# Kernel optimization log

Measured on AMD Instinct MI355X. Metric: run time of the kernel, lower is better.

## Reference

```python
import jax, jax.numpy as jnp
import numpy as np

D = 1024
HEADS = 16
HEAD_DIM = D // HEADS
B = 4
L = 1024


def setup_inputs() -> dict:
    key = jax.random.key(0)
    kq, kk, kv, kw, kb = jax.random.split(key, 5)
    Q = jax.random.normal(kq, (B, L, D), dtype=jnp.float32)
    K = jax.random.normal(kk, (B, L, D), dtype=jnp.float32)
    V = jax.random.normal(kv, (B, L, D), dtype=jnp.float32)
    # Output projection H: torch nn.Linear(D, D) -> weight (D, D), bias (D,)
    lim = 1.0 / np.sqrt(D)
    W_H = jax.random.uniform(kw, (D, D), minval=-lim, maxval=lim, dtype=jnp.float32)
    b_H = jax.random.uniform(kb, (D,), minval=-lim, maxval=lim, dtype=jnp.float32)
    mask = 0  # falsy -> no masking branch, matching `if mask` in the source
    return {"Q": Q, "K": K, "V": V, "W_H": W_H, "b_H": b_H, "mask": mask}


def reference(Q, K, V, W_H, b_H, mask):
    batch, q_len, _ = Q.shape
    k_len = K.shape[1]
    Qh = Q.reshape(batch, q_len, HEADS, HEAD_DIM)
    Kh = K.reshape(batch, k_len, HEADS, HEAD_DIM)
    Vh = V.reshape(batch, k_len, HEADS, HEAD_DIM)
    scores = jnp.einsum('bqhd,bkhd->bhqk', Qh, Kh)  # [B,H,Lq,Lk]
    if mask:  # mask is a Python scalar (0 -> skip), as in source
        scores = jnp.where(mask == 0, -jnp.inf, scores)
    # NOTE: source scales by sqrt(D), not sqrt(head_dim)
    attn = jax.nn.softmax(scores / np.sqrt(D).astype(np.float32), axis=3)
    out = jnp.einsum('bhql,blhd->bqhd', attn, Vh).reshape(batch, q_len, D)
    return out @ W_H.T + b_H
```

## Files before the change

kernel.cpp:

```cpp
#include <hip/hip_runtime.h>
#include <hip/hip_bf16.h>

typedef __attribute__((ext_vector_type(4))) float f32x4;
typedef __attribute__((ext_vector_type(8))) short bf16x8;

constexpr int Bn  = 4;
constexpr int Ln  = 1024;
constexpr int Dn  = 1024;
constexpr int Hn  = 16;
constexpr int HDn = 64;

static __device__ __forceinline__ unsigned short bf16r(float f) {
    union { float f; unsigned int u; } x;
    x.f = f;
    unsigned int r = x.u + 0x7fffu + ((x.u >> 16) & 1u);
    return (unsigned short)(r >> 16);
}

__global__ __launch_bounds__(256) void prep_kernel(
    const float* __restrict__ Kg, const float* __restrict__ Vg,
    const float* __restrict__ Wg, unsigned short* __restrict__ Kbf,
    unsigned short* __restrict__ Vtg, unsigned short* __restrict__ Wbf)
{
    const int tid = threadIdx.x;
    if (blockIdx.z == 4) {
        const int r0 = blockIdx.x * 64, c0 = blockIdx.y * 64;
        for (int i = 0; i < 4; ++i) {
            int e4 = i * 256 + tid;
            int r = e4 >> 4, c4 = e4 & 15;
            const float* p = Wg + (size_t)(r0 + r) * Dn + c0 + c4 * 4;
            float4 v = *(const float4*)p;
            ushort4 o;
            o.x = bf16r(v.x); o.y = bf16r(v.y); o.z = bf16r(v.z); o.w = bf16r(v.w);
            *(ushort4*)(Wbf + (size_t)(r0 + r) * Dn + c0 + c4 * 4) = o;
        }
        return;
    }

    __shared__ unsigned short T[64][72];
    const int k0 = blockIdx.x * 64;
    const int h  = blockIdx.y;
    const int b  = blockIdx.z;
    const float* Kb = Kg + (size_t)b * Ln * Dn + h * HDn;
    const float* Vb = Vg + (size_t)b * Ln * Dn + h * HDn;
    unsigned short* Ko = Kbf + (size_t)b * Ln * Dn + h * HDn;

    for (int i = 0; i < 4; ++i) {
        int e4 = i * 256 + tid;
        int r = e4 >> 4, c4 = e4 & 15;
        float4 kv = *(const float4*)(Kb + (size_t)(k0 + r) * Dn + c4 * 4);
        ushort4 o;
        o.x = bf16r(kv.x); o.y = bf16r(kv.y); o.z = bf16r(kv.z); o.w = bf16r(kv.w);
        *(ushort4*)(Ko + (size_t)(k0 + r) * Dn + c4 * 4) = o;
        float4 vv = *(const float4*)(Vb + (size_t)(k0 + r) * Dn + c4 * 4);
        T[c4 * 4 + 0][r] = bf16r(vv.x);
        T[c4 * 4 + 1][r] = bf16r(vv.y);
        T[c4 * 4 + 2][r] = bf16r(vv.z);
        T[c4 * 4 + 3][r] = bf16r(vv.w);
    }
    __syncthreads();
    unsigned short* out = Vtg + ((size_t)(b * Hn + h) * HDn) * Ln + k0;
    for (int i = 0; i < 2; ++i) {
        int e8 = i * 256 + tid;
        int r = e8 >> 3, c8 = e8 & 7;
        *(uint4*)(out + (size_t)r * Ln + c8 * 8) = *(const uint4*)&T[r][c8 * 8];
    }
}

__global__ __launch_bounds__(512) void attn_kernel(
    const float* __restrict__ Qg, const unsigned short* __restrict__ Kbf,
    const unsigned short* __restrict__ Vtg, unsigned short* __restrict__ Xg)
{
    __shared__ unsigned short Ks[64][72];
    __shared__ unsigned short Vts[64][72];
    __shared__ unsigned short Ps[128][72];

    const int tid  = threadIdx.x;
    const int wave = tid >> 6;
    const int lane = tid & 63;
    const int l16  = lane & 15;
    const int quad = lane >> 4;

    const int q0 = blockIdx.x * 128;
    const int h  = blockIdx.y;
    const int b  = blockIdx.z;

    const unsigned short* Kb16 = Kbf + (size_t)b * Ln * Dn + h * HDn;
    const unsigned short* Vtb  = Vtg + ((size_t)(b * Hn + h) * HDn) * Ln;

    bf16x8 aq0, aq1;
    {
        const float* qp = Qg + ((size_t)b * Ln + q0 + wave * 16 + l16) * Dn
                             + h * HDn + quad * 8;
        float4 a0 = *(const float4*)qp;
        float4 a1 = *(const float4*)(qp + 4);
        float4 a2 = *(const float4*)(qp + 32);
        float4 a3 = *(const float4*)(qp + 36);
        aq0[0] = (short)bf16r(a0.x); aq0[1] = (short)bf16r(a0.y);
        aq0[2] = (short)bf16r(a0.z); aq0[3] = (short)bf16r(a0.w);
        aq0[4] = (short)bf16r(a1.x); aq0[5] = (short)bf16r(a1.y);
        aq0[6] = (short)bf16r(a1.z); aq0[7] = (short)bf16r(a1.w);
        aq1[0] = (short)bf16r(a2.x); aq1[1] = (short)bf16r(a2.y);
        aq1[2] = (short)bf16r(a2.z); aq1[3] = (short)bf16r(a2.w);
        aq1[4] = (short)bf16r(a3.x); aq1[5] = (short)bf16r(a3.y);
        aq1[6] = (short)bf16r(a3.z); aq1[7] = (short)bf16r(a3.w);
    }

    const float SC = 1.4426950408889634f / 32.0f;

    float lsum[4] = {0.f, 0.f, 0.f, 0.f};
    f32x4 Oacc[4];
    for (int d = 0; d < 4; ++d) Oacc[d] = (f32x4){0.f, 0.f, 0.f, 0.f};

    for (int it = 0; it < Ln / 64; ++it) {
        const int k0 = it * 64;
        __syncthreads();
        {
            int r = tid >> 3, c8 = tid & 7;
            *(uint4*)&Ks[r][c8 * 8] =
                *(const uint4*)(Kb16 + (size_t)(k0 + r) * Dn + c8 * 8);
            *(uint4*)&Vts[r][c8 * 8] =
                *(const uint4*)(Vtb + (size_t)r * Ln + k0 + c8 * 8);
        }
        __syncthreads();

        f32x4 s[4];
        for (int n = 0; n < 4; ++n) {
            bf16x8 b0 = *(const bf16x8*)&Ks[n * 16 + l16][quad * 8];
            bf16x8 b1 = *(const bf16x8*)&Ks[n * 16 + l16][32 + quad * 8];
            f32x4 acc = (f32x4){0.f, 0.f, 0.f, 0.f};
            acc = __builtin_amdgcn_mfma_f32_16x16x32_bf16(aq0, b0, acc, 0, 0, 0);
            acc = __builtin_amdgcn_mfma_f32_16x16x32_bf16(aq1, b1, acc, 0, 0, 0);
            s[n] = acc;
        }

        for (int n = 0; n < 4; ++n)
            for (int r = 0; r < 4; ++r) {
                float p = exp2f(s[n][r] * SC);
                s[n][r] = p;
                lsum[r] += p;
            }

        for (int n = 0; n < 4; ++n)
            for (int r = 0; r < 4; ++r)
                Ps[wave * 16 + quad * 4 + r][n * 16 + l16] = bf16r(s[n][r]);

        for (int kk = 0; kk < 2; ++kk) {
            bf16x8 ap = *(const bf16x8*)&Ps[wave * 16 + l16][kk * 32 + quad * 8];
            for (int d = 0; d < 4; ++d) {
                bf16x8 bv = *(const bf16x8*)&Vts[d * 16 + l16][kk * 32 + quad * 8];
                Oacc[d] = __builtin_amdgcn_mfma_f32_16x16x32_bf16(ap, bv, Oacc[d], 0, 0, 0);
            }
        }
    }

    float linv[4];
    for (int r = 0; r < 4; ++r) {
        float rs = lsum[r];
        rs += __shfl_xor(rs, 1, 64);
        rs += __shfl_xor(rs, 2, 64);
        rs += __shfl_xor(rs, 4, 64);
        rs += __shfl_xor(rs, 8, 64);
        linv[r] = 1.f / rs;
    }

    unsigned short* Xb = Xg + ((size_t)b * Ln + q0) * Dn + h * HDn;
    for (int r = 0; r < 4; ++r) {
        int row = wave * 16 + quad * 4 + r;
        for (int d = 0; d < 4; ++d)
            Xb[(size_t)row * Dn + d * 16 + l16] = bf16r(Oacc[d][r] * linv[r]);
    }
}

__global__ __launch_bounds__(256) void proj_kernel(
    const unsigned short* __restrict__ Xg, const unsigned short* __restrict__ Wbf,
    const float* __restrict__ bg, float* __restrict__ Yg)
{
    __shared__ unsigned short Xs[64][136];
    __shared__ unsigned short Wsh[64][136];

    const int tid  = threadIdx.x;
    const int wave = tid >> 6;
    const int lane = tid & 63;
    const int l16  = lane & 15;
    const int quad = lane >> 4;
    const int mw   = (wave & 1) * 32;
    const int nw   = (wave >> 1) * 32;

    const int m0 = blockIdx.x * 64;
    const int n0 = blockIdx.y * 64;

    f32x4 acc[2][2];
    for (int mt = 0; mt < 2; ++mt)
        for (int nt = 0; nt < 2; ++nt)
            acc[mt][nt] = (f32x4){0.f, 0.f, 0.f, 0.f};

    for (int it = 0; it < Dn / 128; ++it) {
        const int kk0 = it * 128;
        __syncthreads();
        for (int i = 0; i < 4; ++i) {
            int idx = i * 256 + tid;
            int r = idx >> 4, c8 = idx & 15;
            *(uint4*)&Xs[r][c8 * 8] =
                *(const uint4*)(Xg + (size_t)(m0 + r) * Dn + kk0 + c8 * 8);
            *(uint4*)&Wsh[r][c8 * 8] =
                *(const uint4*)(Wbf + (size_t)(n0 + r) * Dn + kk0 + c8 * 8);
        }
        __syncthreads();

        for (int kk = 0; kk < 4; ++kk) {
            bf16x8 af[2], bfr[2];
            for (int mt = 0; mt < 2; ++mt)
                af[mt] = *(const bf16x8*)&Xs[mw + mt * 16 + l16][kk * 32 + quad * 8];
            for (int nt = 0; nt < 2; ++nt)
                bfr[nt] = *(const bf16x8*)&Wsh[nw + nt * 16 + l16][kk * 32 + quad * 8];
            for (int mt = 0; mt < 2; ++mt)
                for (int nt = 0; nt < 2; ++nt)
                    acc[mt][nt] = __builtin_amdgcn_mfma_f32_16x16x32_bf16(
                        af[mt], bfr[nt], acc[mt][nt], 0, 0, 0);
        }
    }

    for (int nt = 0; nt < 2; ++nt) {
        int col = n0 + nw + nt * 16 + l16;
        float bb = bg[col];
        for (int mt = 0; mt < 2; ++mt)
            for (int r = 0; r < 4; ++r) {
                int row = m0 + mw + mt * 16 + quad * 4 + r;
                Yg[(size_t)row * Dn + col] = acc[mt][nt][r] + bb;
            }
    }
}

extern "C" void kernel_launch(void* const* d_in, const int* in_sizes, int n_in,
                              void* d_out, int out_size, void* d_ws, size_t ws_size,
                              hipStream_t stream) {
    const float* Q    = (const float*)d_in[0];
    const float* K    = (const float*)d_in[1];
    const float* V    = (const float*)d_in[2];
    const float* W    = (const float*)d_in[3];
    const float* bias = (const float*)d_in[4];

    unsigned short* Kbf = (unsigned short*)d_ws;
    unsigned short* Vt  = Kbf + (size_t)Bn * Ln * Dn;
    unsigned short* Wbf = Vt  + (size_t)Bn * Ln * Dn;
    unsigned short* X   = Wbf + (size_t)Dn * Dn;
    float* Y = (float*)d_out;

    dim3 gp(Ln / 64, Hn, Bn + 1);
    prep_kernel<<<gp, 256, 0, stream>>>(K, V, W, Kbf, Vt, Wbf);

    dim3 g1(Ln / 128, Hn, Bn);
    attn_kernel<<<g1, 512, 0, stream>>>(Q, Kbf, Vt, X);

    dim3 g2((Bn * Ln) / 64, Dn / 64);
    proj_kernel<<<g2, 256, 0, stream>>>(X, Wbf, bias, Y);
}
```

Before: 155.9 us.

## Keep P in registers via transposed QK MFMA; enlarge projection GEMM tiles

The attention kernel swaps the MFMA operands so the score fragments come out laid out as the A operand of a 16x16x16 MFMA. This lets P stay in registers and removes the shared-memory round trip and its bf16 writes, and it packs P to bf16 with perm instructions. The row sum now reduces across quads with fewer shuffles, and the grid order puts heads innermost. The projection GEMM moves to 128x128 tiles with 512 threads and a K step of 64, trading more per-wave accumulators and fewer blocks for more data reuse.

```diff
diff --git a/kernel.cpp b/kernel.cpp
--- a/kernel.cpp
+++ b/kernel.cpp
@@ -3,6 +3,13 @@
 
 typedef __attribute__((ext_vector_type(4))) float f32x4;
 typedef __attribute__((ext_vector_type(8))) short bf16x8;
+typedef __attribute__((ext_vector_type(4))) short bf16x4;
+
+#if __has_builtin(__builtin_amdgcn_mfma_f32_16x16x16_bf16)
+#define MFMA_16x16x16(a, b, c) __builtin_amdgcn_mfma_f32_16x16x16_bf16(a, b, c, 0, 0, 0)
+#else
+#define MFMA_16x16x16(a, b, c) __builtin_amdgcn_mfma_f32_16x16x16bf16_1k(a, b, c, 0, 0, 0)
+#endif
 
 constexpr int Bn  = 4;
 constexpr int Ln  = 1024;
@@ -28,8 +35,7 @@
         for (int i = 0; i < 4; ++i) {
             int e4 = i * 256 + tid;
             int r = e4 >> 4, c4 = e4 & 15;
-            const float* p = Wg + (size_t)(r0 + r) * Dn + c0 + c4 * 4;
-            float4 v = *(const float4*)p;
+            float4 v = *(const float4*)(Wg + (size_t)(r0 + r) * Dn + c0 + c4 * 4);
             ushort4 o;
             o.x = bf16r(v.x); o.y = bf16r(v.y); o.z = bf16r(v.z); o.w = bf16r(v.w);
             *(ushort4*)(Wbf + (size_t)(r0 + r) * Dn + c0 + c4 * 4) = o;
@@ -73,7 +79,6 @@
 {
     __shared__ unsigned short Ks[64][72];
     __shared__ unsigned short Vts[64][72];
-    __shared__ unsigned short Ps[128][72];
 
     const int tid  = threadIdx.x;
     const int wave = tid >> 6;
@@ -81,8 +86,8 @@
     const int l16  = lane & 15;
     const int quad = lane >> 4;
 
-    const int q0 = blockIdx.x * 128;
-    const int h  = blockIdx.y;
+    const int h  = blockIdx.x;
+    const int q0 = blockIdx.y * 128;
     const int b  = blockIdx.z;
 
     const unsigned short* Kb16 = Kbf + (size_t)b * Ln * Dn + h * HDn;
@@ -108,7 +113,7 @@
 
     const float SC = 1.4426950408889634f / 32.0f;
 
-    float lsum[4] = {0.f, 0.f, 0.f, 0.f};
+    float lsum = 0.f;
     f32x4 Oacc[4];
     for (int d = 0; d < 4; ++d) Oacc[d] = (f32x4){0.f, 0.f, 0.f, 0.f};
 
@@ -126,43 +131,43 @@
 
         f32x4 s[4];
         for (int n = 0; n < 4; ++n) {
-            bf16x8 b0 = *(const bf16x8*)&Ks[n * 16 + l16][quad * 8];
-            bf16x8 b1 = *(const bf16x8*)&Ks[n * 16 + l16][32 + quad * 8];
+            bf16x8 ka0 = *(const bf16x8*)&Ks[n * 16 + l16][quad * 8];
+            bf16x8 ka1 = *(const bf16x8*)&Ks[n * 16 + l16][32 + quad * 8];
             f32x4 acc = (f32x4){0.f, 0.f, 0.f, 0.f};
-            acc = __builtin_amdgcn_mfma_f32_16x16x32_bf16(aq0, b0, acc, 0, 0, 0);
-            acc = __builtin_amdgcn_mfma_f32_16x16x32_bf16(aq1, b1, acc, 0, 0, 0);
+            acc = __builtin_amdgcn_mfma_f32_16x16x32_bf16(ka0, aq0, acc, 0, 0, 0);
+            acc = __builtin_amdgcn_mfma_f32_16x16x32_bf16(ka1, aq1, acc, 0, 0, 0);
             s[n] = acc;
         }
 
-        for (int n = 0; n < 4; ++n)
-            for (int r = 0; r < 4; ++r) {
-                float p = exp2f(s[n][r] * SC);
-                s[n][r] = p;
-                lsum[r] += p;
+        bf16x4 pf[4];
+        for (int n = 0; n < 4; ++n) {
+            float p0 = exp2f(s[n][0] * SC);
+            float p1 = exp2f(s[n][1] * SC);
+            float p2 = exp2f(s[n][2] * SC);
+            float p3 = exp2f(s[n][3] * SC);
+            lsum += (p0 + p1) + (p2 + p3);
+            unsigned int u0 = __float_as_uint(p0) + 0x8000u;
+            unsigned int u1 = __float_as_uint(p1) + 0x8000u;
+            unsigned int u2 = __float_as_uint(p2) + 0x8000u;
+            unsigned int u3 = __float_as_uint(p3) + 0x8000u;
+            union { unsigned int u[2]; bf16x4 v; } pk;
+            pk.u[0] = __builtin_amdgcn_perm(u1, u0, 0x07060302u);
+            pk.u[1] = __builtin_amdgcn_perm(u3, u2, 0x07060302u);
+            pf[n] = pk.v;
+        }
+
+        for (int dt = 0; dt < 4; ++dt)
+            for (int kn = 0; kn < 4; ++kn) {
+                bf16x4 bv = *(const bf16x4*)&Vts[dt * 16 + l16][kn * 16 + quad * 4];
+                Oacc[dt] = MFMA_16x16x16(pf[kn], bv, Oacc[dt]);
             }
-
-        for (int n = 0; n < 4; ++n)
-            for (int r = 0; r < 4; ++r)
-                Ps[wave * 16 + quad * 4 + r][n * 16 + l16] = bf16r(s[n][r]);
-
-        for (int kk = 0; kk < 2; ++kk) {
-            bf16x8 ap = *(const bf16x8*)&Ps[wave * 16 + l16][kk * 32 + quad * 8];
-            for (int d = 0; d < 4; ++d) {
-                bf16x8 bv = *(const bf16x8*)&Vts[d * 16 + l16][kk * 32 + quad * 8];
-                Oacc[d] = __builtin_amdgcn_mfma_f32_16x16x32_bf16(ap, bv, Oacc[d], 0, 0, 0);
-            }
-        }
-    }
-
+    }
+
+    lsum += __shfl_xor(lsum, 16, 64);
+    lsum += __shfl_xor(lsum, 32, 64);
     float linv[4];
-    for (int r = 0; r < 4; ++r) {
-        float rs = lsum[r];
-        rs += __shfl_xor(rs, 1, 64);
-        rs += __shfl_xor(rs, 2, 64);
-        rs += __shfl_xor(rs, 4, 64);
-        rs += __shfl_xor(rs, 8, 64);
-        linv[r] = 1.f / rs;
-    }
+    for (int r = 0; r < 4; ++r)
+        linv[r] = 1.f / __shfl(lsum, quad * 4 + r, 64);
 
     unsigned short* Xb = Xg + ((size_t)b * Ln + q0) * Dn + h * HDn;
     for (int r = 0; r < 4; ++r) {
@@ -172,59 +177,63 @@
     }
 }
 
-__global__ __launch_bounds__(256) void proj_kernel(
+__global__ __launch_bounds__(512) void proj_kernel(
     const unsigned short* __restrict__ Xg, const unsigned short* __restrict__ Wbf,
     const float* __restrict__ bg, float* __restrict__ Yg)
 {
-    __shared__ unsigned short Xs[64][136];
-    __shared__ unsigned short Wsh[64][136];
+    __shared__ unsigned short Xs[128][72];
+    __shared__ unsigned short Wsh[128][72];
 
     const int tid  = threadIdx.x;
     const int wave = tid >> 6;
     const int lane = tid & 63;
     const int l16  = lane & 15;
     const int quad = lane >> 4;
-    const int mw   = (wave & 1) * 32;
+    const int mw   = (wave & 1) * 64;
     const int nw   = (wave >> 1) * 32;
 
-    const int m0 = blockIdx.x * 64;
-    const int n0 = blockIdx.y * 64;
-
-    f32x4 acc[2][2];
-    for (int mt = 0; mt < 2; ++mt)
+    const int n0 = blockIdx.x * 128;
+    const int m0 = blockIdx.y * 128;
+
+    f32x4 acc[4][2];
+    for (int mt = 0; mt < 4; ++mt)
         for (int nt = 0; nt < 2; ++nt)
             acc[mt][nt] = (f32x4){0.f, 0.f, 0.f, 0.f};
 
-    for (int it = 0; it < Dn / 128; ++it) {
-        const int kk0 = it * 128;
-        __syncthreads();
-        for (int i = 0; i < 4; ++i) {
-            int idx = i * 256 + tid;
-            int r = idx >> 4, c8 = idx & 15;
-            *(uint4*)&Xs[r][c8 * 8] =
-                *(const uint4*)(Xg + (size_t)(m0 + r) * Dn + kk0 + c8 * 8);
-            *(uint4*)&Wsh[r][c8 * 8] =
-                *(const uint4*)(Wbf + (size_t)(n0 + r) * Dn + kk0 + c8 * 8);
-        }
-        __syncthreads();
-
-        for (int kk = 0; kk < 4; ++kk) {
-            bf16x8 af[2], bfr[2];
-            for (int mt = 0; mt < 2; ++mt)
-                af[mt] = *(const bf16x8*)&Xs[mw + mt * 16 + l16][kk * 32 + quad * 8];
-            for (int nt = 0; nt < 2; ++nt)
-                bfr[nt] = *(const bf16x8*)&Wsh[nw + nt * 16 + l16][kk * 32 + quad * 8];
-            for (int mt = 0; mt < 2; ++mt)
-                for (int nt = 0; nt < 2; ++nt)
-                    acc[mt][nt] = __builtin_amdgcn_mfma_f32_16x16x32_bf16(
-                        af[mt], bfr[nt], acc[mt][nt], 0, 0, 0);
-        }
+    for (int it = 0; it < Dn / 64; ++it) {
+        const int kk0 = it * 64;
+        __syncthreads();
+        {
+            int r = tid >> 3, c8 = tid & 7;
+            const unsigned short* xp = Xg + (size_t)(m0 + r) * Dn + kk0 + c8 * 8;
+            *(uint4*)&Xs[r][c8 * 8]      = *(const uint4*)xp;
+            *(uint4*)&Xs[r + 64][c8 * 8] = *(const uint4*)(xp + (size_t)64 * Dn);
+            const unsigned short* wp = Wbf + (size_t)(n0 + r) * Dn + kk0 + c8 * 8;
+            *(uint4*)&Wsh[r][c8 * 8]      = *(const uint4*)wp;
+            *(uint4*)&Wsh[r + 64][c8 * 8] = *(const uint4*)(wp + (size_t)64 * Dn);
+        }
+        __syncthreads();
+
+        bf16x8 af[4][2], bfr[2][2];
+        for (int mt = 0; mt < 4; ++mt)
+            for (int kk = 0; kk < 2; ++kk)
+                af[mt][kk] = *(const bf16x8*)&Xs[mw + mt * 16 + l16][kk * 32 + quad * 8];
+        for (int nt = 0; nt < 2; ++nt)
+            for (int kk = 0; kk < 2; ++kk)
+                bfr[nt][kk] = *(const bf16x8*)&Wsh[nw + nt * 16 + l16][kk * 32 + quad * 8];
+        for (int mt = 0; mt < 4; ++mt)
+            for (int nt = 0; nt < 2; ++nt) {
+                acc[mt][nt] = __builtin_amdgcn_mfma_f32_16x16x32_bf16(
+                    af[mt][0], bfr[nt][0], acc[mt][nt], 0, 0, 0);
+                acc[mt][nt] = __builtin_amdgcn_mfma_f32_16x16x32_bf16(
+                    af[mt][1], bfr[nt][1], acc[mt][nt], 0, 0, 0);
+            }
     }
 
     for (int nt = 0; nt < 2; ++nt) {
         int col = n0 + nw + nt * 16 + l16;
         float bb = bg[col];
-        for (int mt = 0; mt < 2; ++mt)
+        for (int mt = 0; mt < 4; ++mt)
             for (int r = 0; r < 4; ++r) {
                 int row = m0 + mw + mt * 16 + quad * 4 + r;
                 Yg[(size_t)row * Dn + col] = acc[mt][nt][r] + bb;
@@ -250,9 +259,9 @@
     dim3 gp(Ln / 64, Hn, Bn + 1);
     prep_kernel<<<gp, 256, 0, stream>>>(K, V, W, Kbf, Vt, Wbf);
 
-    dim3 g1(Ln / 128, Hn, Bn);
+    dim3 g1(Hn, Ln / 128, Bn);
     attn_kernel<<<g1, 512, 0, stream>>>(Q, Kbf, Vt, X);
 
-    dim3 g2((Bn * Ln) / 64, Dn / 64);
-    proj_kernel<<<g2, 256, 0, stream>>>(X, Wbf, bias, Y);
-}
+    dim3 g2(Dn / 128, (Bn * Ln) / 128);
+    proj_kernel<<<g2, 512, 0, stream>>>(X, Wbf, bias, Y);
+}
```

Result: no change. 157.1 us (+0.7%).
